# Optimization experiments

Hardware: AMD Instinct MI355X
Metric: run time of the kernel (lower is better)

## Reference

```python
import jax, jax.numpy as jnp
import numpy as np

K = 5
PAD = K // 2
MARGIN = 0.3
EPS_AFF = 1e-9


def setup_inputs() -> dict:
    key = jax.random.key(0)
    k1, k2 = jax.random.split(key)
    pred = jax.random.normal(k1, (4, 64, 192, 640), dtype=jnp.float32)
    target = jax.random.randint(k2, (4, 1, 192, 640), 0, 20, dtype=jnp.int32)
    return {"pred": pred, "target": target}


def _loss_map(pred, target):
    # pred: [B,C,h,w] float, target: [B,1,h,w] int labels (same spatial size
    # as pred, so the nearest-neighbor interpolate in torch is the identity).
    B, C, h, w = pred.shape
    center = target  # [B,1,h,w]
    # label padding uses value=-1 (never matches a real label)
    pad_lbl = jnp.pad(center, ((0, 0), (0, 0), (PAD, PAD), (PAD, PAD)),
                      constant_values=-1)
    # F.normalize(feature, dim=1): x / max(||x||, 1e-12)
    norm = jnp.sqrt(jnp.sum(pred * pred, axis=1, keepdims=True))
    feat = pred / jnp.maximum(norm, 1e-12)
    pad_feat = jnp.pad(feat, ((0, 0), (0, 0), (PAD, PAD), (PAD, PAD)))

    labels, sims = [], []
    for i in range(K):          # fixed 5x5 window, 25 shifted slices
        for j in range(K):
            sh_lbl = pad_lbl[:, :, i:i + h, j:j + w]
            labels.append(center == sh_lbl)
            sh_feat = pad_feat[:, :, i:i + h, j:j + w]
            sims.append(jnp.sum(feat * sh_feat, axis=1, keepdims=True))
    agg = jnp.stack(labels, axis=-1).astype(jnp.float32)  # [B,1,h,w,25]
    sim = jnp.stack(sims, axis=-1)                          # [B,1,h,w,25]

    pos = agg
    neg = 1.0 - agg
    pos_num = jnp.sum(pos, axis=-1)   # [B,1,h,w]; >= 1 (center matches itself)
    neg_num = jnp.sum(neg, axis=-1)
    boundary = (pos_num >= K - 1) & (neg_num >= K - 1)

    affinity = jnp.sqrt(jnp.maximum(EPS_AFF, 2.0 - 2.0 * sim))  # [B,1,h,w,25]
    pos_dist = jnp.sum(pos * affinity, axis=-1) / pos_num
    neg_dist = jnp.sum(neg * affinity, axis=-1) / jnp.maximum(neg_num, 1e-12)

    triplet = jnp.maximum(0.0, pos_dist - neg_dist + MARGIN)
    # torch does boolean indexing loss_map = max(0, ...)[boundary]; we keep the
    # static-shape equivalent: full map zeroed outside the boundary region.
    return jnp.where(boundary, triplet, 0.0)


def reference(pred, target):
    return _loss_map(pred, target)
```

## Files before the change

### kernel.cpp

```cpp
#include <hip/hip_runtime.h>

constexpr int Bn = 4, Cn = 64, Hn = 192, Wn = 640, HW = Hn * Wn;
constexpr int TH = 8, TW = 64;
constexpr int SH = TH + 4;
constexpr int SW = TW + 5;
constexpr int NS = SH * SW;
constexpr int NT = 512;
constexpr int CH = 4;
constexpr int NCHUNK = Cn / CH;
constexpr int DR = SH - 2;
constexpr int ND = DR * SW;
constexpr int NPAIR = (DR / 2) * SW;
constexpr int ARENA = 12 * ND;

__global__ __launch_bounds__(NT, 4) void guide_triplet_kernel(
    const float* __restrict__ pred,
    const int*   __restrict__ target,
    float* __restrict__ out)
{
    __shared__ float arena[ARENA];
    __shared__ float invnS[NS];
    __shared__ int   lblS[NS];

    const int x0 = blockIdx.x * TW;
    const int y0 = blockIdx.y * TH;
    const int b  = blockIdx.z;

    const int tid = threadIdx.x;
    const int tx  = tid & (TW - 1);
    const int ty  = tid >> 6;

    const int e0 = tid;
    const int e1 = tid + NT;
    const bool has1 = (e1 < NS);
    const int r0 = e0 / SW, c0 = e0 % SW;
    const int r1 = e1 / SW, c1 = e1 % SW;
    const int gy0 = y0 + r0 - 2, gx0 = x0 + c0 - 2;
    const int gy1 = y0 + r1 - 2, gx1 = x0 + c1 - 2;
    const bool ok0 = (gy0 >= 0) && (gy0 < Hn) && (gx0 >= 0) && (gx0 < Wn);
    const bool ok1 = has1 && (gy1 >= 0) && (gy1 < Hn) && (gx1 >= 0) && (gx1 < Wn);
    const int off0 = gy0 * Wn + gx0;
    const int off1 = gy1 * Wn + gx1;

    {
        const int* tb = target + b * HW;
        lblS[e0] = ok0 ? tb[off0] : -1;
        if (has1) lblS[e1] = ok1 ? tb[off1] : -1;
    }

    const bool isPair = (tid < NPAIR);
    const int pa = tid / SW;
    const int pc = tid - pa * SW;
    const int rA = 2 * pa;

    float ss0 = 0.0f, ss1 = 0.0f;
    float accA[12], accB[12];
    #pragma unroll
    for (int i = 0; i < 12; ++i) { accA[i] = 0.0f; accB[i] = 0.0f; }

    const float* predb = pred + (size_t)b * Cn * HW;

    float ldA[CH][2], ldB[CH][2];

#define LOADCHUNK(DST, CHUNK) do {                                          \
    _Pragma("unroll")                                                       \
    for (int cc = 0; cc < CH; ++cc) {                                       \
        const float* pc_ = predb + (size_t)((CHUNK) * CH + cc) * HW;        \
        DST[cc][0] = ok0 ? pc_[off0] : 0.0f;                                \
        DST[cc][1] = ok1 ? pc_[off1] : 0.0f;                                \
    } } while (0)

#define BODY(K, LD, KP2) {                                                  \
    float* sb = arena + ((K) & 1) * (CH * NS);                              \
                                         \
    _Pragma("unroll")                                                       \
    for (int cc = 0; cc < CH; ++cc) {                                       \
        sb[cc * NS + e0] = LD[cc][0];                                       \
        ss0 = fmaf(LD[cc][0], LD[cc][0], ss0);                              \
        if (has1) {                                                         \
            sb[cc * NS + e1] = LD[cc][1];                                   \
            ss1 = fmaf(LD[cc][1], LD[cc][1], ss1);                          \
        } }                                                                 \
    __syncthreads();                                                        \
      \
    if ((KP2) < NCHUNK) LOADCHUNK(LD, KP2);                                 \
        \
    if (isPair) {                                                           \
        _Pragma("unroll")                                                   \
        for (int cc = 0; cc < CH; ++cc) {                                   \
            const float* s0 = sb + cc * NS + rA * SW + pc;                  \
            const float w00 = s0[0], w01 = s0[1], w02 = s0[2];              \
            const float* s1 = s0 + (SW - 2);                                \
            const float w10 = s1[0], w11 = s1[1], w12 = s1[2],              \
                        w13 = s1[3], w14 = s1[4];                           \
            const float* s2 = s1 + SW;                                      \
            const float w20 = s2[0], w21 = s2[1], w22 = s2[2],              \
                        w23 = s2[3], w24 = s2[4];                           \
            const float* s3 = s2 + SW;                                      \
            const float w30 = s3[0], w31 = s3[1], w32 = s3[2],              \
                        w33 = s3[3], w34 = s3[4];                           \
            accA[0]  = fmaf(w00, w01, accA[0]);                             \
            accA[1]  = fmaf(w00, w02, accA[1]);                             \
            accA[2]  = fmaf(w00, w10, accA[2]);                             \
            accA[3]  = fmaf(w00, w11, accA[3]);                             \
            accA[4]  = fmaf(w00, w12, accA[4]);                             \
            accA[5]  = fmaf(w00, w13, accA[5]);                             \
            accA[6]  = fmaf(w00, w14, accA[6]);                             \
            accA[7]  = fmaf(w00, w20, accA[7]);                             \
            accA[8]  = fmaf(w00, w21, accA[8]);                             \
            accA[9]  = fmaf(w00, w22, accA[9]);                             \
            accA[10] = fmaf(w00, w23, accA[10]);                            \
            accA[11] = fmaf(w00, w24, accA[11]);                            \
            accB[0]  = fmaf(w12, w13, accB[0]);                             \
            accB[1]  = fmaf(w12, w14, accB[1]);                             \
            accB[2]  = fmaf(w12, w20, accB[2]);                             \
            accB[3]  = fmaf(w12, w21, accB[3]);                             \
            accB[4]  = fmaf(w12, w22, accB[4]);                             \
            accB[5]  = fmaf(w12, w23, accB[5]);                             \
            accB[6]  = fmaf(w12, w24, accB[6]);                             \
            accB[7]  = fmaf(w12, w30, accB[7]);                             \
            accB[8]  = fmaf(w12, w31, accB[8]);                             \
            accB[9]  = fmaf(w12, w32, accB[9]);                             \
            accB[10] = fmaf(w12, w33, accB[10]);                            \
            accB[11] = fmaf(w12, w34, accB[11]);                            \
        } } }

    LOADCHUNK(ldA, 0);
    LOADCHUNK(ldB, 1);

    for (int chunk = 0; chunk < NCHUNK; chunk += 2) {
        BODY(chunk,     ldA, chunk + 2)
        BODY(chunk + 1, ldB, chunk + 3)
    }

    invnS[e0] = 1.0f / fmaxf(sqrtf(ss0), 1e-12f);
    if (has1) invnS[e1] = 1.0f / fmaxf(sqrtf(ss1), 1e-12f);
    __syncthreads();

    if (isPair) {
        const int qA = rA * SW + pc;
        const int qB = qA + SW;
        #pragma unroll
        for (int k = 0; k < 12; ++k) {
            arena[k * ND + qA] = accA[k];
            arena[k * ND + qB] = accB[k];
        }
    }
    __syncthreads();

    const int qp = (2 + ty) * SW + (2 + tx);
    const float ic = invnS[qp];
    const int   lc = lblS[qp];

    float pn = 1.0f, nn = 0.0f, ps = 3.16227766e-5f, ns_ = 0.0f;

    constexpr int DIRD[12] = {1, 2, SW - 2, SW - 1, SW, SW + 1, SW + 2,
                              2 * SW - 2, 2 * SW - 1, 2 * SW, 2 * SW + 1, 2 * SW + 2};
    #pragma unroll
    for (int k = 0; k < 12; ++k) {
        const int dq = DIRD[k];
        {
            const float sim = arena[k * ND + qp] * ic * invnS[qp + dq];
            const float aff = sqrtf(fmaxf(1e-9f, 2.0f - 2.0f * sim));
            const float mf  = (lblS[qp + dq] == lc) ? 1.0f : 0.0f;
            pn += mf; nn += 1.0f - mf;
            ps = fmaf(mf, aff, ps); ns_ = fmaf(1.0f - mf, aff, ns_);
        }
        {
            const float sim = arena[k * ND + qp - dq] * ic * invnS[qp - dq];
            const float aff = sqrtf(fmaxf(1e-9f, 2.0f - 2.0f * sim));
            const float mf  = (lblS[qp - dq] == lc) ? 1.0f : 0.0f;
            pn += mf; nn += 1.0f - mf;
            ps = fmaf(mf, aff, ps); ns_ = fmaf(1.0f - mf, aff, ns_);
        }
    }
    const bool boundary = (pn >= 4.0f) && (nn >= 4.0f);
    const float tri = fmaxf(0.0f, ps / pn - ns_ / fmaxf(nn, 1e-12f) + 0.3f);
    out[((size_t)b * Hn + (y0 + ty)) * Wn + (x0 + tx)] = boundary ? tri : 0.0f;
}

extern "C" void kernel_launch(void* const* d_in, const int* in_sizes, int n_in,
                              void* d_out, int out_size, void* d_ws, size_t ws_size,
                              hipStream_t stream) {
    const float* pred   = (const float*)d_in[0];
    const int*   target = (const int*)d_in[1];
    float*       out    = (float*)d_out;
    dim3 grid(Wn / TW, Hn / TH, Bn);
    guide_triplet_kernel<<<grid, NT, 0, stream>>>(pred, target, out);
}
```

Baseline: 72.32 us.

## Vectorize halo loads as float2 pairs and precompute affinities per pair

```diff
diff --git a/kernel.cpp b/kernel.cpp
--- a/kernel.cpp
+++ b/kernel.cpp
@@ -3,8 +3,10 @@
 constexpr int Bn = 4, Cn = 64, Hn = 192, Wn = 640, HW = Hn * Wn;
 constexpr int TH = 8, TW = 64;
 constexpr int SH = TH + 4;
-constexpr int SW = TW + 5;
+constexpr int SW = TW + 4;
 constexpr int NS = SH * SW;
+constexpr int NP = NS / 2;
+constexpr int PPR = SW / 2;
 constexpr int NT = 512;
 constexpr int CH = 4;
 constexpr int NCHUNK = Cn / CH;
@@ -19,7 +21,7 @@
     float* __restrict__ out)
 {
     __shared__ float arena[ARENA];
-    __shared__ float invnS[NS];
+    __shared__ float invnS[NS + 4];
     __shared__ int   lblS[NS];
 
     const int x0 = blockIdx.x * TW;
@@ -30,59 +32,62 @@
     const int tx  = tid & (TW - 1);
     const int ty  = tid >> 6;
 
-    const int e0 = tid;
-    const int e1 = tid + NT;
-    const bool has1 = (e1 < NS);
-    const int r0 = e0 / SW, c0 = e0 % SW;
-    const int r1 = e1 / SW, c1 = e1 % SW;
-    const int gy0 = y0 + r0 - 2, gx0 = x0 + c0 - 2;
-    const int gy1 = y0 + r1 - 2, gx1 = x0 + c1 - 2;
-    const bool ok0 = (gy0 >= 0) && (gy0 < Hn) && (gx0 >= 0) && (gx0 < Wn);
-    const bool ok1 = has1 && (gy1 >= 0) && (gy1 < Hn) && (gx1 >= 0) && (gx1 < Wn);
-    const int off0 = gy0 * Wn + gx0;
-    const int off1 = gy1 * Wn + gx1;
+    const bool hasS = (tid < NP);
+    const int srow = tid / PPR;
+    const int spc  = tid - srow * PPR;
+    const int gy = y0 + srow - 2;
+    const int gx = x0 + 2 * spc - 2;
+    const bool okS = hasS && (gy >= 0) && (gy < Hn) && (gx >= 0) && (gx + 1 < Wn);
+    const int goff = gy * Wn + gx;
+    const int sidx = 2 * tid;
 
-    {
-        const int* tb = target + b * HW;
-        lblS[e0] = ok0 ? tb[off0] : -1;
-        if (has1) lblS[e1] = ok1 ? tb[off1] : -1;
+    if (hasS) {
+        int lx = -1, ly = -1;
+        if (okS) {
+            const int2 L = *reinterpret_cast<const int2*>(target + b * HW + goff);
+            lx = L.x; ly = L.y;
+        }
+        lblS[sidx]     = lx;
+        lblS[sidx + 1] = ly;
     }
+    if (tid < 4) invnS[NS + tid] = 1.0f;
 
     const bool isPair = (tid < NPAIR);
     const int pa = tid / SW;
     const int pc = tid - pa * SW;
     const int rA = 2 * pa;
 
-    float ss0 = 0.0f, ss1 = 0.0f;
+    float ssx = 0.0f, ssy = 0.0f;
     float accA[12], accB[12];
     #pragma unroll
     for (int i = 0; i < 12; ++i) { accA[i] = 0.0f; accB[i] = 0.0f; }
 
     const float* predb = pred + (size_t)b * Cn * HW;
 
-    float ldA[CH][2], ldB[CH][2];
+    float2 ldA[CH], ldB[CH];
 
 #define LOADCHUNK(DST, CHUNK) do {                                          \
     _Pragma("unroll")                                                       \
     for (int cc = 0; cc < CH; ++cc) {                                       \
         const float* pc_ = predb + (size_t)((CHUNK) * CH + cc) * HW;        \
-        DST[cc][0] = ok0 ? pc_[off0] : 0.0f;                                \
-        DST[cc][1] = ok1 ? pc_[off1] : 0.0f;                                \
+        float2 v = make_float2(0.f, 0.f);                                   \
+        if (okS) v = *reinterpret_cast<const float2*>(pc_ + goff);          \
+        DST[cc] = v;                                                        \
     } } while (0)
 
 #define BODY(K, LD, KP2) {                                                  \
     float* sb = arena + ((K) & 1) * (CH * NS);                              \
-                                         \
-    _Pragma("unroll")                                                       \
-    for (int cc = 0; cc < CH; ++cc) {                                       \
-        sb[cc * NS + e0] = LD[cc][0];                                       \
-        ss0 = fmaf(LD[cc][0], LD[cc][0], ss0);                              \
-        if (has1) {                                                         \
-            sb[cc * NS + e1] = LD[cc][1];                                   \
-            ss1 = fmaf(LD[cc][1], LD[cc][1], ss1);                          \
+                          \
+    if (hasS) {                                                             \
+        _Pragma("unroll")                                                   \
+        for (int cc = 0; cc < CH; ++cc) {                                   \
+            const float2 v = LD[cc];                                        \
+            *reinterpret_cast<float2*>(&sb[cc * NS + sidx]) = v;            \
+            ssx = fmaf(v.x, v.x, ssx);                                      \
+            ssy = fmaf(v.y, v.y, ssy);                                      \
         } }                                                                 \
     __syncthreads();                                                        \
-      \
+                         \
     if ((KP2) < NCHUNK) LOADCHUNK(LD, KP2);                                 \
         \
     if (isPair) {                                                           \
@@ -133,49 +138,53 @@
         BODY(chunk + 1, ldB, chunk + 3)
     }
 
-    invnS[e0] = 1.0f / fmaxf(sqrtf(ss0), 1e-12f);
-    if (has1) invnS[e1] = 1.0f / fmaxf(sqrtf(ss1), 1e-12f);
+    if (hasS) {
+        invnS[sidx]     = 1.0f / fmaxf(sqrtf(ssx), 1e-12f);
+        invnS[sidx + 1] = 1.0f / fmaxf(sqrtf(ssy), 1e-12f);
+    }
     __syncthreads();
+
+    constexpr int DIRD[12] = {1, 2, SW - 2, SW - 1, SW, SW + 1, SW + 2,
+                              2 * SW - 2, 2 * SW - 1, 2 * SW, 2 * SW + 1, 2 * SW + 2};
 
     if (isPair) {
         const int qA = rA * SW + pc;
         const int qB = qA + SW;
+        const float icA = invnS[qA];
+        const float icB = invnS[qB];
         #pragma unroll
         for (int k = 0; k < 12; ++k) {
-            arena[k * ND + qA] = accA[k];
-            arena[k * ND + qB] = accB[k];
+            const int dq = DIRD[k];
+            const float simA = accA[k] * icA * invnS[qA + dq];
+            const float simB = accB[k] * icB * invnS[qB + dq];
+            arena[k * ND + qA] = sqrtf(fmaxf(1e-9f, fmaf(-2.0f, simA, 2.0f)));
+            arena[k * ND + qB] = sqrtf(fmaxf(1e-9f, fmaf(-2.0f, simB, 2.0f)));
         }
     }
     __syncthreads();
 
     const int qp = (2 + ty) * SW + (2 + tx);
-    const float ic = invnS[qp];
-    const int   lc = lblS[qp];
+    const int lc = lblS[qp];
 
-    float pn = 1.0f, nn = 0.0f, ps = 3.16227766e-5f, ns_ = 0.0f;
-
-    constexpr int DIRD[12] = {1, 2, SW - 2, SW - 1, SW, SW + 1, SW + 2,
-                              2 * SW - 2, 2 * SW - 1, 2 * SW, 2 * SW + 1, 2 * SW + 2};
+    float tot = 0.0f, ps = 0.0f, pn = 0.0f;
     #pragma unroll
     for (int k = 0; k < 12; ++k) {
         const int dq = DIRD[k];
-        {
-            const float sim = arena[k * ND + qp] * ic * invnS[qp + dq];
-            const float aff = sqrtf(fmaxf(1e-9f, 2.0f - 2.0f * sim));
-            const float mf  = (lblS[qp + dq] == lc) ? 1.0f : 0.0f;
-            pn += mf; nn += 1.0f - mf;
-            ps = fmaf(mf, aff, ps); ns_ = fmaf(1.0f - mf, aff, ns_);
-        }
-        {
-            const float sim = arena[k * ND + qp - dq] * ic * invnS[qp - dq];
-            const float aff = sqrtf(fmaxf(1e-9f, 2.0f - 2.0f * sim));
-            const float mf  = (lblS[qp - dq] == lc) ? 1.0f : 0.0f;
-            pn += mf; nn += 1.0f - mf;
-            ps = fmaf(mf, aff, ps); ns_ = fmaf(1.0f - mf, aff, ns_);
-        }
+        const float affF = arena[k * ND + qp];
+        const float affB = arena[k * ND + qp - dq];
+        const float mfF = (lblS[qp + dq] == lc) ? 1.0f : 0.0f;
+        const float mfB = (lblS[qp - dq] == lc) ? 1.0f : 0.0f;
+        tot += affF + affB;
+        pn += mfF + mfB;
+        ps = fmaf(mfF, affF, fmaf(mfB, affB, ps));
     }
-    const bool boundary = (pn >= 4.0f) && (nn >= 4.0f);
-    const float tri = fmaxf(0.0f, ps / pn - ns_ / fmaxf(nn, 1e-12f) + 0.3f);
+    const float pos_num = pn + 1.0f;
+    const float pos_sum = ps + 3.16227766e-5f;
+    const float neg_num = 24.0f - pn;
+    const float neg_sum = tot - ps;
+    const bool boundary = (pos_num >= 4.0f) && (neg_num >= 4.0f);
+    const float tri = fmaxf(0.0f,
+        pos_sum / pos_num - neg_sum / fmaxf(neg_num, 1e-12f) + 0.3f);
     out[((size_t)b * Hn + (y0 + ty)) * Wn + (x0 + tx)] = boundary ? tri : 0.0f;
 }
 
```

Result: faster. 67.66 us (-6.5%).
